# Performance work log

Measured on AMD Instinct MI355X. Metric: run time of the kernel, lower is better.

The kernel has to match this reference:

```python
import jax, jax.numpy as jnp
import numpy as np

NUM_HEADS = 32
NUM_KV_HEADS = 8
HEAD_DIM = 128
HIDDEN = 4096
RANK = 8
ALPHA = 16.0
SCALING = ALPHA / RANK
EPS = 1e-8


def dora_linear(x, W, A, B, m):
    # DoRA: W_eff = W + scaling * B @ A; directional component normalized per
    # output row, rescaled by learned magnitude m.
    W_eff = W + SCALING * (B @ A)                      # [out, in]
    norm = jnp.linalg.norm(W_eff, axis=1)              # [out]
    W_d = W_eff * (m / (norm + EPS))[:, None]
    return x @ W_d.T


def setup_inputs() -> dict:
    key = jax.random.key(0)
    ks = jax.random.split(key, 16)
    B_, S = 2, 2048
    hidden_states = jax.random.normal(ks[0], (B_, S, HIDDEN), jnp.float32)
    # additive causal mask
    causal = jnp.triu(jnp.full((S, S), -1e9, jnp.float32), k=1)
    attention_mask = jnp.broadcast_to(causal, (B_, 1, S, S))

    def w(k, shape, scale=0.02):
        return scale * jax.random.normal(k, shape, jnp.float32)

    Wq = w(ks[1], (HIDDEN, HIDDEN)); Aq = w(ks[2], (RANK, HIDDEN)); Bq = w(ks[3], (HIDDEN, RANK))
    Wk = w(ks[4], (NUM_KV_HEADS * HEAD_DIM, HIDDEN)); Ak = w(ks[5], (RANK, HIDDEN)); Bk = w(ks[6], (NUM_KV_HEADS * HEAD_DIM, RANK))
    Wv = w(ks[7], (NUM_KV_HEADS * HEAD_DIM, HIDDEN)); Av = w(ks[8], (RANK, HIDDEN)); Bv = w(ks[9], (NUM_KV_HEADS * HEAD_DIM, RANK))
    Wo = w(ks[10], (HIDDEN, HIDDEN)); Ao = w(ks[11], (RANK, HIDDEN)); Bo = w(ks[12], (HIDDEN, RANK))
    # DoRA magnitude init: column-norm of base weight (per output row)
    mq = jnp.linalg.norm(Wq, axis=1)
    mk = jnp.linalg.norm(Wk, axis=1)
    mv = jnp.linalg.norm(Wv, axis=1)
    mo = jnp.linalg.norm(Wo, axis=1)
    return dict(hidden_states=hidden_states, attention_mask=attention_mask,
                Wq=Wq, Aq=Aq, Bq=Bq, mq=mq,
                Wk=Wk, Ak=Ak, Bk=Bk, mk=mk,
                Wv=Wv, Av=Av, Bv=Bv, mv=mv,
                Wo=Wo, Ao=Ao, Bo=Bo, mo=mo)


def reference(hidden_states, attention_mask,
              Wq, Aq, Bq, mq, Wk, Ak, Bk, mk,
              Wv, Av, Bv, mv, Wo, Ao, Bo, mo):
    bsz, q_len, _ = hidden_states.shape
    n_rep = NUM_HEADS // NUM_KV_HEADS

    q = dora_linear(hidden_states, Wq, Aq, Bq, mq)
    k = dora_linear(hidden_states, Wk, Ak, Bk, mk)
    v = dora_linear(hidden_states, Wv, Av, Bv, mv)

    q = q.reshape(bsz, q_len, NUM_HEADS, HEAD_DIM).transpose(0, 2, 1, 3)
    k = k.reshape(bsz, q_len, NUM_KV_HEADS, HEAD_DIM).transpose(0, 2, 1, 3)
    v = v.reshape(bsz, q_len, NUM_KV_HEADS, HEAD_DIM).transpose(0, 2, 1, 3)

    # _apply_rotary_pos_emb is a no-op in the source: (q, k) unchanged

    # repeat_kv for grouped-query attention
    k = jnp.repeat(k, n_rep, axis=1)  # [b, H, s, d]
    v = jnp.repeat(v, n_rep, axis=1)

    scale = 1.0 / jnp.sqrt(jnp.float32(HEAD_DIM))
    attn_weights = jnp.einsum('bhqd,bhkd->bhqk', q, k) * scale
    attn_weights = attn_weights + attention_mask
    attn_weights = jax.nn.softmax(attn_weights, axis=-1)
    attn_output = jnp.einsum('bhqk,bhkd->bhqd', attn_weights, v)
    attn_output = attn_output.transpose(0, 2, 1, 3).reshape(bsz, q_len, HIDDEN)
    attn_output = dora_linear(attn_output, Wo, Ao, Bo, mo)
    return attn_output
```

## Files before the change

### kernel.cpp

```cpp
#include <hip/hip_runtime.h>
#include <hip/hip_bf16.h>
#include <stdint.h>

#define HIDDEN 4096
#define RANK   8
#define SCALING 2.0f
#define EPS    1e-8f
#define SEQ    2048
#define BATCH  2
#define NH     32
#define NKVH   8
#define HD     128
#define MROWS  (BATCH*SEQ)
#define NQKV   6144

typedef __attribute__((ext_vector_type(8))) short bf16x8;
typedef __attribute__((ext_vector_type(4))) short bf16x4;
typedef __attribute__((ext_vector_type(4))) float f32x4;

__device__ __forceinline__ void gload_lds16(const void* g, void* lds) {
  __builtin_amdgcn_global_load_lds((__attribute__((address_space(1))) void*)g,
                                   (__attribute__((address_space(3))) void*)lds,
                                   16, 0, 0);
}

__device__ __forceinline__ unsigned short f2bf(float f) {
  __hip_bfloat16 h = __float2bfloat16(f);
  return *reinterpret_cast<unsigned short*>(&h);
}

__device__ __forceinline__ void store_c(float* p, float v) { *p = v; }
__device__ __forceinline__ void store_c(__hip_bfloat16* p, float v) { *p = __float2bfloat16(v); }

__device__ __forceinline__ bf16x8 lds_read8_b64(const short* p) {
  bf16x4 lo = *(const bf16x4*)p;
  bf16x4 hi = *(const bf16x4*)(p + 4);
  bf16x8 r;
  r[0]=lo[0]; r[1]=lo[1]; r[2]=lo[2]; r[3]=lo[3];
  r[4]=hi[0]; r[5]=hi[1]; r[6]=hi[2]; r[7]=hi[3];
  return r;
}

__launch_bounds__(256)
__global__ void cast_kernel(const float* __restrict__ x, unsigned short* __restrict__ y) {
  const size_t i = ((size_t)blockIdx.x * 256 + threadIdx.x) * 4;
  const float4 v = *(const float4*)&x[i];
  ushort4 pk;
  pk.x = f2bf(v.x); pk.y = f2bf(v.y); pk.z = f2bf(v.z); pk.w = f2bf(v.w);
  *(ushort4*)&y[i] = pk;
}

__launch_bounds__(256)
__global__ void wd_kernel(const float* __restrict__ W, const float* __restrict__ A,
                          const float* __restrict__ B, const float* __restrict__ m,
                          unsigned short* __restrict__ out) {
  const int row = blockIdx.x;
  const int tid = threadIdx.x;
  float bl[RANK];
#pragma unroll
  for (int t = 0; t < RANK; ++t) bl[t] = SCALING * B[row*RANK + t];
  float ev[16];
  float ss = 0.f;
#pragma unroll
  for (int it = 0; it < 4; ++it) {
    const int j = it*1024 + tid*4;
    const float4 wv = *(const float4*)&W[(size_t)row*HIDDEN + j];
    float e0 = wv.x, e1 = wv.y, e2 = wv.z, e3 = wv.w;
#pragma unroll
    for (int t = 0; t < RANK; ++t) {
      const float4 av = *(const float4*)&A[t*HIDDEN + j];
      e0 += bl[t]*av.x; e1 += bl[t]*av.y; e2 += bl[t]*av.z; e3 += bl[t]*av.w;
    }
    ev[it*4+0]=e0; ev[it*4+1]=e1; ev[it*4+2]=e2; ev[it*4+3]=e3;
    ss += e0*e0 + e1*e1 + e2*e2 + e3*e3;
  }
#pragma unroll
  for (int off = 32; off > 0; off >>= 1) ss += __shfl_down(ss, off, 64);
  __shared__ float wsum[4];
  if ((tid & 63) == 0) wsum[tid >> 6] = ss;
  __syncthreads();
  const float norm = sqrtf(wsum[0]+wsum[1]+wsum[2]+wsum[3]);
  const float scl = m[row] / (norm + EPS);
#pragma unroll
  for (int it = 0; it < 4; ++it) {
    const int j = it*1024 + tid*4;
    ushort4 pk;
    pk.x = f2bf(ev[it*4+0]*scl); pk.y = f2bf(ev[it*4+1]*scl);
    pk.z = f2bf(ev[it*4+2]*scl); pk.w = f2bf(ev[it*4+3]*scl);
    *(ushort4*)&out[(size_t)row*HIDDEN + j] = pk;
  }
}

template<typename CT>
__launch_bounds__(256)
__global__ void gemm_bt(const __hip_bfloat16* __restrict__ A,
                        const __hip_bfloat16* __restrict__ B,
                        CT* __restrict__ C, const int M, const int N, const int K) {
  __shared__ __hip_bfloat16 As[128*64];
  __shared__ __hip_bfloat16 Bs[128*64];
  const int tid = threadIdx.x;
  const int w = tid >> 6, l = tid & 63;
  const int tM = blockIdx.y * 128, tN = blockIdx.x * 128;
  const int wm = (w >> 1) * 64, wn = (w & 1) * 64;
  const int lr = l >> 3;
  const int lcs = ((l & 7) ^ lr) * 8;
  const int q4 = l >> 4;
  const int ln = l & 15;
  const int sw = ln & 7;
  f32x4 acc[4][4] = {};
  const __hip_bfloat16* Ab = A + (size_t)tM * K;
  const __hip_bfloat16* Bb = B + (size_t)tN * K;
  for (int k0 = 0; k0 < K; k0 += 64) {
    __syncthreads();
#pragma unroll
    for (int i = 0; i < 4; ++i) {
      const int rr = i*32 + w*8;
      gload_lds16(Ab + (size_t)(rr + lr)*K + (k0 + lcs), &As[rr*64]);
      gload_lds16(Bb + (size_t)(rr + lr)*K + (k0 + lcs), &Bs[rr*64]);
    }
    __syncthreads();
    const short* Ap = (const short*)As;
    const short* Bp = (const short*)Bs;
#pragma unroll
    for (int ks = 0; ks < 2; ++ks) {
      const int slot = ((ks*4 + q4) ^ sw) * 8;
      bf16x8 af[4], bff[4];
#pragma unroll
      for (int mi = 0; mi < 4; ++mi)
        af[mi] = *(const bf16x8*)&Ap[(wm + mi*16 + ln)*64 + slot];
#pragma unroll
      for (int ni = 0; ni < 4; ++ni)
        bff[ni] = *(const bf16x8*)&Bp[(wn + ni*16 + ln)*64 + slot];
#pragma unroll
      for (int mi = 0; mi < 4; ++mi)
#pragma unroll
        for (int ni = 0; ni < 4; ++ni)
          acc[mi][ni] = __builtin_amdgcn_mfma_f32_16x16x32_bf16(af[mi], bff[ni], acc[mi][ni], 0, 0, 0);
    }
  }
  const int r0 = tM + wm + q4*4;
  const int c0 = tN + wn + ln;
#pragma unroll
  for (int mi = 0; mi < 4; ++mi)
#pragma unroll
    for (int ni = 0; ni < 4; ++ni)
#pragma unroll
      for (int r = 0; r < 4; ++r)
        store_c(&C[(size_t)(r0 + mi*16 + r)*N + c0 + ni*16], acc[mi][ni][r]);
}

#define VT_S 68
#define PS_S 68
__launch_bounds__(256, 3)
__global__ void attn_kernel(const __hip_bfloat16* __restrict__ qkv,
                            __hip_bfloat16* __restrict__ out) {
  const int bid = blockIdx.x;
  const int qt = 31 - (bid >> 6);
  const int hb = bid & 63;
  const int h  = hb & 31;
  const int b  = hb >> 5;
  const int kvh = h >> 2;
  const int tid = threadIdx.x;
  const int w = tid >> 6, l = tid & 63;
  const int q4 = l >> 4;
  const int ln = l & 15;
  const int sw = ln & 7;

  __shared__ __hip_bfloat16 Ks[64*128];
  __shared__ __hip_bfloat16 Vt[128*VT_S];
  __shared__ __hip_bfloat16 Ps[4][16*PS_S];

  const __hip_bfloat16* kb = qkv + (size_t)(b*SEQ)*NQKV + HIDDEN + kvh*HD;
  const __hip_bfloat16* vb = qkv + (size_t)(b*SEQ)*NQKV + (HIDDEN+1024) + kvh*HD;

  const int krow = l >> 4;
  const int kchunk = ((l & 15) ^ krow ^ ((w & 1) << 2)) * 8;

  bf16x8 aq[4];
  {
    const __hip_bfloat16* qr = qkv + (size_t)(b*SEQ + qt*64 + w*16 + ln)*NQKV + h*HD;
#pragma unroll
    for (int ks = 0; ks < 4; ++ks) {
      uint4 raw = *(const uint4*)(qr + ks*32 + q4*8);
      aq[ks] = *(const bf16x8*)&raw;
    }
  }

  f32x4 o[8] = {};
  float mrow[4] = {-1e30f,-1e30f,-1e30f,-1e30f};
  float lrow[4] = {0.f,0.f,0.f,0.f};
  const float sc = 0.08838834764831845f;

  const int nkv = qt + 1;
  for (int j = 0; j < nkv; ++j) {
    __syncthreads();
#pragma unroll
    for (int i = 0; i < 4; ++i) {
      const int rr = i*16 + w*4;
      gload_lds16(kb + (size_t)(j*64 + rr + krow)*NQKV + kchunk, &Ks[rr*128]);
    }
#pragma unroll
    for (int it = 0; it < 4; ++it) {
      const int chunk = it*256 + tid;
      const int kv = chunk & 63;
      const int d0 = (chunk >> 6) * 8;
      uint4 raw = *(const uint4*)(vb + (size_t)(j*64 + kv)*NQKV + d0);
      const __hip_bfloat16* pv = (const __hip_bfloat16*)&raw;
#pragma unroll
      for (int t = 0; t < 8; ++t) Vt[(d0 + t)*VT_S + kv] = pv[t];
    }
    __syncthreads();

    f32x4 s[4] = {};
    const short* Kp = (const short*)Ks;
#pragma unroll
    for (int ks = 0; ks < 4; ++ks) {
      const int slot = ((ks*4 + q4) ^ sw) * 8;
#pragma unroll
      for (int nt = 0; nt < 4; ++nt) {
        bf16x8 bk = *(const bf16x8*)&Kp[(nt*16 + ln)*128 + slot];
        s[nt] = __builtin_amdgcn_mfma_f32_16x16x32_bf16(aq[ks], bk, s[nt], 0, 0, 0);
      }
    }

    float p[4][4];
#pragma unroll
    for (int r = 0; r < 4; ++r) {
      float mx = mrow[r];
#pragma unroll
      for (int nt = 0; nt < 4; ++nt) {
        float v = s[nt][r] * sc;
        if (j == qt) {
          const int qrow = w*16 + q4*4 + r;
          const int kvc = nt*16 + ln;
          if (kvc > qrow) v = -1e30f;
        }
        p[r][nt] = v;
        mx = fmaxf(mx, v);
      }
#pragma unroll
      for (int d = 1; d < 16; d <<= 1) mx = fmaxf(mx, __shfl_xor(mx, d, 64));
      const float alpha = __expf(mrow[r] - mx);
      float rs = 0.f;
#pragma unroll
      for (int nt = 0; nt < 4; ++nt) { const float e = __expf(p[r][nt] - mx); p[r][nt] = e; rs += e; }
#pragma unroll
      for (int d = 1; d < 16; d <<= 1) rs += __shfl_xor(rs, d, 64);
      mrow[r] = mx;
      lrow[r] = lrow[r]*alpha + rs;
#pragma unroll
      for (int ni = 0; ni < 8; ++ni) o[ni][r] *= alpha;
    }

    __hip_bfloat16* Pw = Ps[w];
#pragma unroll
    for (int r = 0; r < 4; ++r)
#pragma unroll
      for (int nt = 0; nt < 4; ++nt)
        Pw[(q4*4 + r)*PS_S + nt*16 + ln] = __float2bfloat16(p[r][nt]);

    const short* Pp = (const short*)Ps[w];
    const short* Vp = (const short*)Vt;
#pragma unroll
    for (int ks = 0; ks < 2; ++ks) {
      bf16x8 ap = lds_read8_b64(&Pp[ln*PS_S + ks*32 + q4*8]);
#pragma unroll
      for (int ni = 0; ni < 8; ++ni) {
        bf16x8 bv = lds_read8_b64(&Vp[(ni*16 + ln)*VT_S + ks*32 + q4*8]);
        o[ni] = __builtin_amdgcn_mfma_f32_16x16x32_bf16(ap, bv, o[ni], 0, 0, 0);
      }
    }
  }

  const int row0 = b*SEQ + qt*64 + w*16 + q4*4;
#pragma unroll
  for (int r = 0; r < 4; ++r) {
    const float inv = 1.f / lrow[r];
#pragma unroll
    for (int ni = 0; ni < 8; ++ni)
      out[(size_t)(row0 + r)*HIDDEN + h*HD + ni*16 + ln] = __float2bfloat16(o[ni][r] * inv);
  }
}

extern "C" void kernel_launch(void* const* d_in, const int* in_sizes, int n_in,
                              void* d_out, int out_size, void* d_ws, size_t ws_size,
                              hipStream_t stream) {
  (void)in_sizes; (void)n_in; (void)out_size; (void)ws_size;
  const float* x  = (const float*)d_in[0];
  const float* Wq = (const float*)d_in[2];
  const float* Aq = (const float*)d_in[3];
  const float* Bq = (const float*)d_in[4];
  const float* mq = (const float*)d_in[5];
  const float* Wk = (const float*)d_in[6];
  const float* Ak = (const float*)d_in[7];
  const float* Bk = (const float*)d_in[8];
  const float* mk = (const float*)d_in[9];
  const float* Wv = (const float*)d_in[10];
  const float* Av = (const float*)d_in[11];
  const float* Bv = (const float*)d_in[12];
  const float* mv = (const float*)d_in[13];
  const float* Wo = (const float*)d_in[14];
  const float* Ao = (const float*)d_in[15];
  const float* Bo = (const float*)d_in[16];
  const float* mo = (const float*)d_in[17];

  char* ws = (char*)d_ws;
  __hip_bfloat16* xbf = (__hip_bfloat16*)ws;
  __hip_bfloat16* wd  = (__hip_bfloat16*)(ws + (size_t)33554432);
  __hip_bfloat16* qkv = (__hip_bfloat16*)(ws + (size_t)83886080);

  cast_kernel<<<16384, 256, 0, stream>>>(x, (unsigned short*)xbf);
  wd_kernel<<<4096, 256, 0, stream>>>(Wq, Aq, Bq, mq, (unsigned short*)wd);
  wd_kernel<<<1024, 256, 0, stream>>>(Wk, Ak, Bk, mk, (unsigned short*)(wd + (size_t)4096*4096));
  wd_kernel<<<1024, 256, 0, stream>>>(Wv, Av, Bv, mv, (unsigned short*)(wd + (size_t)5120*4096));
  gemm_bt<__hip_bfloat16><<<dim3(48, 32), 256, 0, stream>>>(xbf, wd, qkv, MROWS, NQKV, HIDDEN);
  wd_kernel<<<4096, 256, 0, stream>>>(Wo, Ao, Bo, mo, (unsigned short*)wd);
  attn_kernel<<<2048, 256, 0, stream>>>(qkv, xbf);
  gemm_bt<float><<<dim3(32, 32), 256, 0, stream>>>(xbf, wd, (float*)d_out, MROWS, HIDDEN, HIDDEN);
}
```

Before: 901.0 us.

## Fuse prep kernels and process two query tiles per attention block

Merges the input cast and all four DoRA weight-normalization launches into one prep kernel, using a separate workspace slot for the Wo weights when the workspace is large enough. The attention kernel now handles 128 query rows per block as two 64-row halves that share each K/V tile load, halving K/V traffic and the grid size. It also computes S transposed (K as the A operand), so the softmax reductions use only two cross-lane shuffles, and it transposes V into LDS with vectorized 4-wide stores. The trade-off is higher register pressure from doubled accumulators, which may lower occupancy, and fewer blocks to balance the causal workload.

```diff
diff --git a/kernel.cpp b/kernel.cpp
--- a/kernel.cpp
+++ b/kernel.cpp
@@ -41,21 +41,10 @@
   return r;
 }
 
-__launch_bounds__(256)
-__global__ void cast_kernel(const float* __restrict__ x, unsigned short* __restrict__ y) {
-  const size_t i = ((size_t)blockIdx.x * 256 + threadIdx.x) * 4;
-  const float4 v = *(const float4*)&x[i];
-  ushort4 pk;
-  pk.x = f2bf(v.x); pk.y = f2bf(v.y); pk.z = f2bf(v.z); pk.w = f2bf(v.w);
-  *(ushort4*)&y[i] = pk;
-}
-
-__launch_bounds__(256)
-__global__ void wd_kernel(const float* __restrict__ W, const float* __restrict__ A,
-                          const float* __restrict__ B, const float* __restrict__ m,
-                          unsigned short* __restrict__ out) {
-  const int row = blockIdx.x;
-  const int tid = threadIdx.x;
+__device__ __forceinline__ void wd_row(const float* __restrict__ W, const float* __restrict__ A,
+                                       const float* __restrict__ B, const float* __restrict__ m,
+                                       unsigned short* __restrict__ out, int row, int tid,
+                                       float* wsum) {
   float bl[RANK];
 #pragma unroll
   for (int t = 0; t < RANK; ++t) bl[t] = SCALING * B[row*RANK + t];
@@ -76,7 +65,6 @@
   }
 #pragma unroll
   for (int off = 32; off > 0; off >>= 1) ss += __shfl_down(ss, off, 64);
-  __shared__ float wsum[4];
   if ((tid & 63) == 0) wsum[tid >> 6] = ss;
   __syncthreads();
   const float norm = sqrtf(wsum[0]+wsum[1]+wsum[2]+wsum[3]);
@@ -89,6 +77,40 @@
     pk.z = f2bf(ev[it*4+2]*scl); pk.w = f2bf(ev[it*4+3]*scl);
     *(ushort4*)&out[(size_t)row*HIDDEN + j] = pk;
   }
+}
+
+__launch_bounds__(256)
+__global__ void prep_kernel(const float* __restrict__ x, unsigned short* __restrict__ xbf,
+                            const float* Wq, const float* Aq, const float* Bq, const float* mq, unsigned short* wdq,
+                            const float* Wk, const float* Ak, const float* Bk, const float* mk, unsigned short* wdk,
+                            const float* Wv, const float* Av, const float* Bv, const float* mv, unsigned short* wdv,
+                            const float* Wo, const float* Ao, const float* Bo, const float* mo, unsigned short* wdo) {
+  __shared__ float wsum[4];
+  const int bid = blockIdx.x;
+  const int tid = threadIdx.x;
+  if (bid < 16384) {
+    const size_t i = ((size_t)bid * 256 + tid) * 4;
+    const float4 v = *(const float4*)&x[i];
+    ushort4 pk;
+    pk.x = f2bf(v.x); pk.y = f2bf(v.y); pk.z = f2bf(v.z); pk.w = f2bf(v.w);
+    *(ushort4*)&xbf[i] = pk;
+  } else if (bid < 20480) {
+    wd_row(Wq, Aq, Bq, mq, wdq, bid - 16384, tid, wsum);
+  } else if (bid < 21504) {
+    wd_row(Wk, Ak, Bk, mk, wdk, bid - 20480, tid, wsum);
+  } else if (bid < 22528) {
+    wd_row(Wv, Av, Bv, mv, wdv, bid - 21504, tid, wsum);
+  } else {
+    wd_row(Wo, Ao, Bo, mo, wdo, bid - 22528, tid, wsum);
+  }
+}
+
+__launch_bounds__(256)
+__global__ void wd_kernel(const float* __restrict__ W, const float* __restrict__ A,
+                          const float* __restrict__ B, const float* __restrict__ m,
+                          unsigned short* __restrict__ out) {
+  __shared__ float wsum[4];
+  wd_row(W, A, B, m, out, blockIdx.x, threadIdx.x, wsum);
 }
 
 template<typename CT>
@@ -155,7 +177,7 @@
 __global__ void attn_kernel(const __hip_bfloat16* __restrict__ qkv,
                             __hip_bfloat16* __restrict__ out) {
   const int bid = blockIdx.x;
-  const int qt = 31 - (bid >> 6);
+  const int qt = 15 - (bid >> 6);
   const int hb = bid & 63;
   const int h  = hb & 31;
   const int b  = hb >> 5;
@@ -168,50 +190,63 @@
 
   __shared__ __hip_bfloat16 Ks[64*128];
   __shared__ __hip_bfloat16 Vt[128*VT_S];
-  __shared__ __hip_bfloat16 Ps[4][16*PS_S];
+  __shared__ __hip_bfloat16 Ps[4][2][16*PS_S];
 
   const __hip_bfloat16* kb = qkv + (size_t)(b*SEQ)*NQKV + HIDDEN + kvh*HD;
   const __hip_bfloat16* vb = qkv + (size_t)(b*SEQ)*NQKV + (HIDDEN+1024) + kvh*HD;
 
+  const int Q0 = qt*128;
+
   const int krow = l >> 4;
   const int kchunk = ((l & 15) ^ krow ^ ((w & 1) << 2)) * 8;
 
-  bf16x8 aq[4];
-  {
-    const __hip_bfloat16* qr = qkv + (size_t)(b*SEQ + qt*64 + w*16 + ln)*NQKV + h*HD;
+  const int vc4 = (tid & 15) * 4;
+  const int vd0 = (tid >> 4) * 8;
+
+  bf16x8 aq[2][4];
+#pragma unroll
+  for (int hf = 0; hf < 2; ++hf) {
+    const __hip_bfloat16* qr = qkv + (size_t)(b*SEQ + Q0 + hf*64 + w*16 + ln)*NQKV + h*HD;
 #pragma unroll
     for (int ks = 0; ks < 4; ++ks) {
       uint4 raw = *(const uint4*)(qr + ks*32 + q4*8);
-      aq[ks] = *(const bf16x8*)&raw;
-    }
-  }
-
-  f32x4 o[8] = {};
-  float mrow[4] = {-1e30f,-1e30f,-1e30f,-1e30f};
-  float lrow[4] = {0.f,0.f,0.f,0.f};
+      aq[hf][ks] = *(const bf16x8*)&raw;
+    }
+  }
+
+  f32x4 o[2][8] = {};
+  float mx[2] = {-1e30f, -1e30f};
+  float lsum[2] = {0.f, 0.f};
   const float sc = 0.08838834764831845f;
-
-  const int nkv = qt + 1;
-  for (int j = 0; j < nkv; ++j) {
+  const int qabs0 = Q0 + w*16 + ln;
+
+  const int jmax = 2*qt + 1;
+  for (int j = 0; j <= jmax; ++j) {
+    const int do0 = (j <= 2*qt);
     __syncthreads();
 #pragma unroll
     for (int i = 0; i < 4; ++i) {
       const int rr = i*16 + w*4;
       gload_lds16(kb + (size_t)(j*64 + rr + krow)*NQKV + kchunk, &Ks[rr*128]);
     }
-#pragma unroll
-    for (int it = 0; it < 4; ++it) {
-      const int chunk = it*256 + tid;
-      const int kv = chunk & 63;
-      const int d0 = (chunk >> 6) * 8;
-      uint4 raw = *(const uint4*)(vb + (size_t)(j*64 + kv)*NQKV + d0);
-      const __hip_bfloat16* pv = (const __hip_bfloat16*)&raw;
-#pragma unroll
-      for (int t = 0; t < 8; ++t) Vt[(d0 + t)*VT_S + kv] = pv[t];
+    {
+      uint4 r0 = *(const uint4*)(vb + (size_t)(j*64 + vc4 + 0)*NQKV + vd0);
+      uint4 r1 = *(const uint4*)(vb + (size_t)(j*64 + vc4 + 1)*NQKV + vd0);
+      uint4 r2 = *(const uint4*)(vb + (size_t)(j*64 + vc4 + 2)*NQKV + vd0);
+      uint4 r3 = *(const uint4*)(vb + (size_t)(j*64 + vc4 + 3)*NQKV + vd0);
+      const unsigned short* p0 = (const unsigned short*)&r0;
+      const unsigned short* p1 = (const unsigned short*)&r1;
+      const unsigned short* p2 = (const unsigned short*)&r2;
+      const unsigned short* p3 = (const unsigned short*)&r3;
+#pragma unroll
+      for (int t = 0; t < 8; ++t) {
+        ushort4 pk; pk.x = p0[t]; pk.y = p1[t]; pk.z = p2[t]; pk.w = p3[t];
+        *(ushort4*)&Vt[(vd0 + t)*VT_S + vc4] = pk;
+      }
     }
     __syncthreads();
 
-    f32x4 s[4] = {};
+    f32x4 s[2][4] = {};
     const short* Kp = (const short*)Ks;
 #pragma unroll
     for (int ks = 0; ks < 4; ++ks) {
@@ -219,73 +254,94 @@
 #pragma unroll
       for (int nt = 0; nt < 4; ++nt) {
         bf16x8 bk = *(const bf16x8*)&Kp[(nt*16 + ln)*128 + slot];
-        s[nt] = __builtin_amdgcn_mfma_f32_16x16x32_bf16(aq[ks], bk, s[nt], 0, 0, 0);
-      }
-    }
-
-    float p[4][4];
-#pragma unroll
-    for (int r = 0; r < 4; ++r) {
-      float mx = mrow[r];
+        if (do0) s[0][nt] = __builtin_amdgcn_mfma_f32_16x16x32_bf16(bk, aq[0][ks], s[0][nt], 0, 0, 0);
+        s[1][nt] = __builtin_amdgcn_mfma_f32_16x16x32_bf16(bk, aq[1][ks], s[1][nt], 0, 0, 0);
+      }
+    }
+
+#pragma unroll
+    for (int hf = 0; hf < 2; ++hf) {
+      if (hf == 0 && !do0) continue;
+      const int qabs = qabs0 + hf*64;
+      if (j == 2*qt + hf) {
+#pragma unroll
+        for (int nt = 0; nt < 4; ++nt)
+#pragma unroll
+          for (int r = 0; r < 4; ++r) {
+            const int kvabs = j*64 + nt*16 + q4*4 + r;
+            if (kvabs > qabs) s[hf][nt][r] = -1e30f;
+          }
+      }
+      float vmax = mx[hf];
+#pragma unroll
+      for (int nt = 0; nt < 4; ++nt)
+#pragma unroll
+        for (int r = 0; r < 4; ++r) vmax = fmaxf(vmax, s[hf][nt][r]);
+      vmax = fmaxf(vmax, __shfl_xor(vmax, 16, 64));
+      vmax = fmaxf(vmax, __shfl_xor(vmax, 32, 64));
+      const float alpha = __expf((mx[hf] - vmax) * sc);
+      float rs = 0.f;
+#pragma unroll
+      for (int nt = 0; nt < 4; ++nt)
+#pragma unroll
+        for (int r = 0; r < 4; ++r) {
+          const float e = __expf((s[hf][nt][r] - vmax) * sc);
+          s[hf][nt][r] = e; rs += e;
+        }
+      rs += __shfl_xor(rs, 16, 64);
+      rs += __shfl_xor(rs, 32, 64);
+      mx[hf] = vmax;
+      lsum[hf] = lsum[hf]*alpha + rs;
+#pragma unroll
+      for (int r = 0; r < 4; ++r) {
+        const float ar = __shfl(alpha, q4*4 + r, 64);
+#pragma unroll
+        for (int ni = 0; ni < 8; ++ni) o[hf][ni][r] *= ar;
+      }
+      __hip_bfloat16* Pw = Ps[w][hf];
 #pragma unroll
       for (int nt = 0; nt < 4; ++nt) {
-        float v = s[nt][r] * sc;
-        if (j == qt) {
-          const int qrow = w*16 + q4*4 + r;
-          const int kvc = nt*16 + ln;
-          if (kvc > qrow) v = -1e30f;
-        }
-        p[r][nt] = v;
-        mx = fmaxf(mx, v);
-      }
-#pragma unroll
-      for (int d = 1; d < 16; d <<= 1) mx = fmaxf(mx, __shfl_xor(mx, d, 64));
-      const float alpha = __expf(mrow[r] - mx);
-      float rs = 0.f;
-#pragma unroll
-      for (int nt = 0; nt < 4; ++nt) { const float e = __expf(p[r][nt] - mx); p[r][nt] = e; rs += e; }
-#pragma unroll
-      for (int d = 1; d < 16; d <<= 1) rs += __shfl_xor(rs, d, 64);
-      mrow[r] = mx;
-      lrow[r] = lrow[r]*alpha + rs;
-#pragma unroll
-      for (int ni = 0; ni < 8; ++ni) o[ni][r] *= alpha;
-    }
-
-    __hip_bfloat16* Pw = Ps[w];
-#pragma unroll
-    for (int r = 0; r < 4; ++r)
-#pragma unroll
-      for (int nt = 0; nt < 4; ++nt)
-        Pw[(q4*4 + r)*PS_S + nt*16 + ln] = __float2bfloat16(p[r][nt]);
-
-    const short* Pp = (const short*)Ps[w];
+        ushort4 pk;
+        pk.x = f2bf(s[hf][nt][0]); pk.y = f2bf(s[hf][nt][1]);
+        pk.z = f2bf(s[hf][nt][2]); pk.w = f2bf(s[hf][nt][3]);
+        *(ushort4*)&Pw[ln*PS_S + nt*16 + q4*4] = pk;
+      }
+    }
+
     const short* Vp = (const short*)Vt;
+    const short* Pp0 = (const short*)Ps[w][0];
+    const short* Pp1 = (const short*)Ps[w][1];
 #pragma unroll
     for (int ks = 0; ks < 2; ++ks) {
-      bf16x8 ap = lds_read8_b64(&Pp[ln*PS_S + ks*32 + q4*8]);
+      bf16x8 ap0 = lds_read8_b64(&Pp0[ln*PS_S + ks*32 + q4*8]);
+      bf16x8 ap1 = lds_read8_b64(&Pp1[ln*PS_S + ks*32 + q4*8]);
 #pragma unroll
       for (int ni = 0; ni < 8; ++ni) {
         bf16x8 bv = lds_read8_b64(&Vp[(ni*16 + ln)*VT_S + ks*32 + q4*8]);
-        o[ni] = __builtin_amdgcn_mfma_f32_16x16x32_bf16(ap, bv, o[ni], 0, 0, 0);
-      }
-    }
-  }
-
-  const int row0 = b*SEQ + qt*64 + w*16 + q4*4;
-#pragma unroll
-  for (int r = 0; r < 4; ++r) {
-    const float inv = 1.f / lrow[r];
-#pragma unroll
-    for (int ni = 0; ni < 8; ++ni)
-      out[(size_t)(row0 + r)*HIDDEN + h*HD + ni*16 + ln] = __float2bfloat16(o[ni][r] * inv);
+        if (do0) o[0][ni] = __builtin_amdgcn_mfma_f32_16x16x32_bf16(ap0, bv, o[0][ni], 0, 0, 0);
+        o[1][ni] = __builtin_amdgcn_mfma_f32_16x16x32_bf16(ap1, bv, o[1][ni], 0, 0, 0);
+      }
+    }
+  }
+
+#pragma unroll
+  for (int hf = 0; hf < 2; ++hf) {
+    const int row0 = b*SEQ + Q0 + hf*64 + w*16 + q4*4;
+#pragma unroll
+    for (int r = 0; r < 4; ++r) {
+      const float lr = __shfl(lsum[hf], q4*4 + r, 64);
+      const float inv = 1.f / lr;
+#pragma unroll
+      for (int ni = 0; ni < 8; ++ni)
+        out[(size_t)(row0 + r)*HIDDEN + h*HD + ni*16 + ln] = __float2bfloat16(o[hf][ni][r] * inv);
+    }
   }
 }
 
 extern "C" void kernel_launch(void* const* d_in, const int* in_sizes, int n_in,
                               void* d_out, int out_size, void* d_ws, size_t ws_size,
                               hipStream_t stream) {
-  (void)in_sizes; (void)n_in; (void)out_size; (void)ws_size;
+  (void)in_sizes; (void)n_in; (void)out_size;
   const float* x  = (const float*)d_in[0];
   const float* Wq = (const float*)d_in[2];
   const float* Aq = (const float*)d_in[3];
@@ -308,13 +364,18 @@
   __hip_bfloat16* xbf = (__hip_bfloat16*)ws;
   __hip_bfloat16* wd  = (__hip_bfloat16*)(ws + (size_t)33554432);
   __hip_bfloat16* qkv = (__hip_bfloat16*)(ws + (size_t)83886080);
-
-  cast_kernel<<<16384, 256, 0, stream>>>(x, (unsigned short*)xbf);
-  wd_kernel<<<4096, 256, 0, stream>>>(Wq, Aq, Bq, mq, (unsigned short*)wd);
-  wd_kernel<<<1024, 256, 0, stream>>>(Wk, Ak, Bk, mk, (unsigned short*)(wd + (size_t)4096*4096));
-  wd_kernel<<<1024, 256, 0, stream>>>(Wv, Av, Bv, mv, (unsigned short*)(wd + (size_t)5120*4096));
+  const bool big = ws_size >= (size_t)167772160;
+  __hip_bfloat16* wdo = big ? (__hip_bfloat16*)(ws + (size_t)134217728) : wd;
+
+  prep_kernel<<<big ? 26624 : 22528, 256, 0, stream>>>(
+      x, (unsigned short*)xbf,
+      Wq, Aq, Bq, mq, (unsigned short*)wd,
+      Wk, Ak, Bk, mk, (unsigned short*)(wd + (size_t)4096*4096),
+      Wv, Av, Bv, mv, (unsigned short*)(wd + (size_t)5120*4096),
+      Wo, Ao, Bo, mo, (unsigned short*)wdo);
   gemm_bt<__hip_bfloat16><<<dim3(48, 32), 256, 0, stream>>>(xbf, wd, qkv, MROWS, NQKV, HIDDEN);
-  wd_kernel<<<4096, 256, 0, stream>>>(Wo, Ao, Bo, mo, (unsigned short*)wd);
-  attn_kernel<<<2048, 256, 0, stream>>>(qkv, xbf);
-  gemm_bt<float><<<dim3(32, 32), 256, 0, stream>>>(xbf, wd, (float*)d_out, MROWS, HIDDEN, HIDDEN);
-}
+  if (!big)
+    wd_kernel<<<4096, 256, 0, stream>>>(Wo, Ao, Bo, mo, (unsigned short*)wdo);
+  attn_kernel<<<1024, 256, 0, stream>>>(qkv, xbf);
+  gemm_bt<float><<<dim3(32, 32), 256, 0, stream>>>(xbf, wdo, (float*)d_out, MROWS, HIDDEN, HIDDEN);
+}
```

Result: faster. 819.1 us (-9.1%).
